# Optimization experiments

Measured on AMD Instinct MI355X. Metric: run time of the kernel, lower is better.

Reference implementation:

```python
import jax, jax.numpy as jnp
import numpy as np

VOCAB = 100000
TAGS = 48
EMB = 256
HID = 512
B, S = 64, 512


def setup_inputs() -> dict:
    key = jax.random.key(0)
    ks = jax.random.split(key, 7)
    sc_e = 1.0 / np.sqrt(EMB)
    sc_h = 1.0 / np.sqrt(HID)
    return {
        "x": jax.random.randint(ks[0], (B, S), 0, VOCAB),
        "emb": jax.random.normal(ks[1], (VOCAB, EMB), jnp.float32),
        "W_ih": jax.random.uniform(ks[2], (4 * HID, EMB), jnp.float32, -sc_e, sc_e),
        "W_hh": jax.random.uniform(ks[3], (4 * HID, HID), jnp.float32, -sc_h, sc_h),
        "b_hh": jax.random.uniform(ks[4], (4 * HID,), jnp.float32, -sc_h, sc_h),
        "fc_W": jax.random.uniform(ks[5], (TAGS, HID), jnp.float32, -sc_h, sc_h),
        "fc_b": jax.random.uniform(ks[6], (TAGS,), jnp.float32, -sc_h, sc_h),
    }


def reference(x, emb, W_ih, W_hh, b_hh, fc_W, fc_b):
    # Embedding lookup: [B,S] -> [B,S,E]
    xe = emb[x]
    # Precompute input projection for all timesteps: [B,S,4H]
    px = jnp.einsum("bse,ge->bsg", xe, W_ih)
    H = W_hh.shape[1]
    Bc = x.shape[0]
    h0 = jnp.zeros((Bc, H), px.dtype)
    c0 = jnp.zeros((Bc, H), px.dtype)

    def step(carry, pxt):
        h, c = carry
        # recurrent dropout prob = 0 -> mask is identity
        gates = pxt + h @ W_hh.T + b_hh  # [B,4H]
        i, f, g, o = jnp.split(gates, 4, axis=-1)
        i = jax.nn.sigmoid(i)
        f = jax.nn.sigmoid(f)
        g = jnp.tanh(g)
        o = jax.nn.sigmoid(o)
        c = f * c + i * g
        h = o * jnp.tanh(c)
        return (h, c), h

    _, hs = jax.lax.scan(step, (h0, c0), jnp.swapaxes(px, 0, 1))
    hs = jnp.swapaxes(hs, 0, 1)  # [B,S,H]
    logits = hs @ fc_W.T + fc_b  # [B,S,TAGS]
    return jax.nn.log_softmax(logits, axis=2)
```

## Files before the change

kernel.cpp:

```cpp
#include <hip/hip_runtime.h>
#include <hip/hip_bf16.h>
#include <hip/hip_fp16.h>

typedef __attribute__((ext_vector_type(8))) short short8;
typedef __attribute__((ext_vector_type(4))) float f32x4;
typedef __attribute__((ext_vector_type(4))) unsigned int u32x4;

#define Hh 512
#define Bb 64
#define Ss 512
#define Gg 2048
#define NROW 32768

static __device__ inline short f2bf(float f) {
    union { float f; unsigned u; } v; v.f = f;
    unsigned r = (v.u + 0x7FFFu + ((v.u >> 16) & 1u)) >> 16;
    return (short)r;
}

static __device__ inline short8 pack_bf8(const float* p) {
    f32x4 u0 = *(const f32x4*)p;
    f32x4 u1 = *(const f32x4*)(p + 4);
    short8 t;
    t[0] = f2bf(u0[0]); t[1] = f2bf(u0[1]); t[2] = f2bf(u0[2]); t[3] = f2bf(u0[3]);
    t[4] = f2bf(u1[0]); t[5] = f2bf(u1[1]); t[6] = f2bf(u1[2]); t[7] = f2bf(u1[3]);
    return t;
}

static __device__ inline float fsigmoid(float x) {
    return __builtin_amdgcn_rcpf(1.f + __builtin_amdgcn_exp2f(x * -1.44269504088896f));
}
static __device__ inline float ftanh(float x) {
    float xc = fminf(fmaxf(x, -15.f), 15.f);
    float e = __builtin_amdgcn_exp2f(xc * 2.88539008177793f);
    return (e - 1.f) / (e + 1.f);
}

__global__ __launch_bounds__(256)
void prep_bf16(const float* __restrict__ wih, const float* __restrict__ fcw,
               short* __restrict__ wih_bf, short* __restrict__ fcw_bf) {
    const int n1 = Gg * 256;
    const int n2 = 48 * Hh;
    for (int i = blockIdx.x * blockDim.x + threadIdx.x; i < n1 + n2;
         i += gridDim.x * blockDim.x) {
        if (i < n1) wih_bf[i] = f2bf(wih[i]);
        else        fcw_bf[i - n1] = f2bf(fcw[i - n1]);
    }
}

__global__ __launch_bounds__(256)
void px_kernel(const int* __restrict__ x, const float* __restrict__ emb,
               const short* __restrict__ wih_bf, const float* __restrict__ bhh,
               _Float16* __restrict__ px) {
    const int w = threadIdx.x >> 6, lane = threadIdx.x & 63;
    const int lr = lane & 15, lc = lane >> 4;
    const int r0 = blockIdx.x * 64 + w * 16;

    short8 a[8];
    const int tok = x[r0 + lr];
    const float* arow = emb + (long)tok * 256;
#pragma unroll
    for (int ks = 0; ks < 8; ks++)
        a[ks] = pack_bf8(arow + ks * 32 + lc * 8);

    for (int g0 = 0; g0 < Gg; g0 += 16) {
        f32x4 acc = {0.f, 0.f, 0.f, 0.f};
#pragma unroll
        for (int ks = 0; ks < 8; ks++) {
            short8 b = *(const short8*)(wih_bf + (g0 + lr) * 256 + ks * 32 + lc * 8);
            acc = __builtin_amdgcn_mfma_f32_16x16x32_bf16(a[ks], b, acc, 0, 0, 0);
        }
        const float bias = bhh[g0 + lr];
#pragma unroll
        for (int i = 0; i < 4; i++) {
            const int r = r0 + lc * 4 + i;
            const int bb = r >> 9, s = r & 511;
            px[((long)s * Bb + bb) * Gg + g0 + lr] = (_Float16)(acc[i] + bias);
        }
    }
}

__global__ __launch_bounds__(512)
void lstm_kernel(const float* __restrict__ whh, const _Float16* __restrict__ px,
                 unsigned int* __restrict__ hbuf32,
                 unsigned int* __restrict__ hs32,
                 int* __restrict__ flags) {
    const int cl  = blockIdx.x & 3;
    const int wgc = blockIdx.x >> 2;
    const int b0 = cl * 16;
    const int J0 = wgc * 64;
    const int tid = threadIdx.x;
    const int w = tid >> 6;
    const int lane = tid & 63;
    const int lr = lane & 15, lc = lane >> 4;
    const int gt = w & 3;
    const int Jsub = (w >> 2) * 32;

    __shared__ float gates[4][16][66];
    __shared__ __align__(16) unsigned int hlds[16 * 256];

    short8 wf[2][16];
#pragma unroll
    for (int u = 0; u < 2; u++)
#pragma unroll
        for (int ks = 0; ks < 16; ks++)
            wf[u][ks] = pack_bf8(whh + (long)(gt * Hh + J0 + Jsub + u * 16 + lr) * Hh + ks * 32 + lc * 8);

    const int eb = tid >> 5;
    const int jp = tid & 31;
    float c0 = 0.f, c1 = 0.f;

    const int gr0 = gt * Hh + J0 + Jsub + lr;

    const int srow = tid >> 5;
    const int scg  = tid & 31;
    const int q0c  = 2 * scg;
    const int chi0 = (q0c ^ ((q0c >> 3) & 7) ^ (srow & 7));
    const int sidx0 = srow * 256 + chi0 * 4;
    const int sidx1 = srow * 256 + (chi0 ^ 1) * 4;

    int* const myflag = flags + cl * 32 + wgc;
    const int* const pollbase = flags + cl * 32;

    float pfA[2][4], pfB[2][4];
#pragma unroll
    for (int u = 0; u < 2; u++)
#pragma unroll
        for (int i = 0; i < 4; i++)
            pfA[u][i] = (float)px[((long)0 * Bb + b0 + lc * 4 + i) * Gg + gr0 + u * 16];

#define LSTM_STEP(T, PFU, PFN)                                                         \
    {                                                                                  \
        const int T_ = (T);                                                            \
        if (T_ == 0) {                                                                 \
            u32x4 z = {0u, 0u, 0u, 0u};                                                \
            *(u32x4*)&hlds[sidx0] = z;                                                 \
            *(u32x4*)&hlds[sidx1] = z;                                                 \
        } else {                                                                       \
            const int* fp = pollbase + (lane & 7);                                     \
            int fv = __hip_atomic_load(fp, __ATOMIC_RELAXED, __HIP_MEMORY_SCOPE_AGENT);\
            while (__any(fv < T_))                                                     \
                fv = __hip_atomic_load(fp, __ATOMIC_RELAXED, __HIP_MEMORY_SCOPE_AGENT);\
            asm volatile("" ::: "memory");                                             \
            const unsigned long long* hb = (const unsigned long long*)                 \
                (hbuf32 + (T_ & 1) * (Bb * Hh / 2) + (b0 + srow) * 256 + scg * 8);     \
            unsigned long long a0 = __hip_atomic_load(hb + 0, __ATOMIC_RELAXED, __HIP_MEMORY_SCOPE_AGENT); \
            unsigned long long a1 = __hip_atomic_load(hb + 1, __ATOMIC_RELAXED, __HIP_MEMORY_SCOPE_AGENT); \
            unsigned long long a2 = __hip_atomic_load(hb + 2, __ATOMIC_RELAXED, __HIP_MEMORY_SCOPE_AGENT); \
            unsigned long long a3 = __hip_atomic_load(hb + 3, __ATOMIC_RELAXED, __HIP_MEMORY_SCOPE_AGENT); \
            u32x4 v0 = {(unsigned)a0, (unsigned)(a0 >> 32), (unsigned)a1, (unsigned)(a1 >> 32)}; \
            u32x4 v1 = {(unsigned)a2, (unsigned)(a2 >> 32), (unsigned)a3, (unsigned)(a3 >> 32)}; \
            *(u32x4*)&hlds[sidx0] = v0;                                                \
            *(u32x4*)&hlds[sidx1] = v1;                                                \
        }                                                                              \
        __syncthreads();                                         \
        f32x4 acc0, acc1;                                                              \
        _Pragma("unroll")                                                              \
        for (int i = 0; i < 4; i++) { acc0[i] = PFU[0][i]; acc1[i] = PFU[1][i]; }      \
        _Pragma("unroll")                                                              \
        for (int ks = 0; ks < 16; ks++) {                                              \
            const int q = ks * 4 + lc;                                                 \
            const int chi = q ^ ((q >> 3) & 7) ^ (lr & 7);                             \
            const short8 af = *(const short8*)&hlds[lr * 256 + chi * 4];               \
            acc0 = __builtin_amdgcn_mfma_f32_16x16x32_bf16(af, wf[0][ks], acc0, 0, 0, 0); \
            acc1 = __builtin_amdgcn_mfma_f32_16x16x32_bf16(af, wf[1][ks], acc1, 0, 0, 0); \
        }                                                                              \
        _Pragma("unroll")                                                              \
        for (int i = 0; i < 4; i++) {                                                  \
            gates[gt][lc * 4 + i][Jsub + lr]      = acc0[i];                           \
            gates[gt][lc * 4 + i][Jsub + 16 + lr] = acc1[i];                           \
        }                                                                              \
        __syncthreads();                                           \
        unsigned hpack;                                                                \
        {                                                                              \
            const float2 gI = *(const float2*)&gates[0][eb][jp * 2];                   \
            const float2 gF = *(const float2*)&gates[1][eb][jp * 2];                   \
            const float2 gG = *(const float2*)&gates[2][eb][jp * 2];                   \
            const float2 gO = *(const float2*)&gates[3][eb][jp * 2];                   \
            c0 = fsigmoid(gF.x) * c0 + fsigmoid(gI.x) * ftanh(gG.x);                   \
            c1 = fsigmoid(gF.y) * c1 + fsigmoid(gI.y) * ftanh(gG.y);                   \
            const float h0 = fsigmoid(gO.x) * ftanh(c0);                               \
            const float h1 = fsigmoid(gO.y) * ftanh(c1);                               \
            hpack = (unsigned)(unsigned short)f2bf(h0)                                 \
                  | ((unsigned)(unsigned short)f2bf(h1) << 16);                        \
            unsigned int* hw = hbuf32 + ((T_ + 1) & 1) * (Bb * Hh / 2)                 \
                               + (b0 + eb) * 256 + (J0 >> 1) + jp;                     \
            __hip_atomic_store(hw, hpack, __ATOMIC_RELAXED, __HIP_MEMORY_SCOPE_AGENT); \
        }                                                                              \
        __syncthreads();          \
        if (tid == 0)                                                                  \
            __hip_atomic_store(myflag, T_ + 1, __ATOMIC_RELAXED, __HIP_MEMORY_SCOPE_AGENT); \
        hs32[((long)(b0 + eb) * Ss + T_) * 256 + (J0 >> 1) + jp] = hpack;              \
        const int tn = (T_ + 1 < Ss) ? T_ + 1 : T_;                                    \
        _Pragma("unroll")                                                              \
        for (int u = 0; u < 2; u++)                                                    \
            _Pragma("unroll")                                                          \
            for (int i = 0; i < 4; i++)                                                \
                PFN[u][i] = (float)px[((long)tn * Bb + b0 + lc * 4 + i) * Gg + gr0 + u * 16]; \
    }

#pragma unroll 1
    for (int t = 0; t < Ss; t += 2) {
        LSTM_STEP(t,     pfA, pfB)
        LSTM_STEP(t + 1, pfB, pfA)
    }
#undef LSTM_STEP
}

__global__ __launch_bounds__(256)
void fc_kernel(const unsigned short* __restrict__ hs, const short* __restrict__ fcw_bf,
               const float* __restrict__ fcb, float* __restrict__ out) {
    const int w = threadIdx.x >> 6, lane = threadIdx.x & 63;
    const int lr = lane & 15, lc = lane >> 4;
    const int r0 = blockIdx.x * 64 + w * 16;

    short8 af[16];
#pragma unroll
    for (int ks = 0; ks < 16; ks++)
        af[ks] = *(const short8*)((const short*)hs + (long)(r0 + lr) * Hh + ks * 32 + lc * 8);

    f32x4 acc[3];
#pragma unroll
    for (int nt = 0; nt < 3; nt++) {
        f32x4 a_ = {0.f, 0.f, 0.f, 0.f};
#pragma unroll
        for (int ks = 0; ks < 16; ks++) {
            short8 b = *(const short8*)(fcw_bf + (nt * 16 + lr) * Hh + ks * 32 + lc * 8);
            a_ = __builtin_amdgcn_mfma_f32_16x16x32_bf16(af[ks], b, a_, 0, 0, 0);
        }
        acc[nt] = a_;
    }

    const float bb0 = fcb[lr], bb1 = fcb[16 + lr], bb2 = fcb[32 + lr];
#pragma unroll
    for (int i = 0; i < 4; i++) {
        float v0 = acc[0][i] + bb0, v1 = acc[1][i] + bb1, v2 = acc[2][i] + bb2;
        float m = fmaxf(v0, fmaxf(v1, v2));
#pragma unroll
        for (int d = 1; d < 16; d <<= 1) m = fmaxf(m, __shfl_xor(m, d));
        float s = expf(v0 - m) + expf(v1 - m) + expf(v2 - m);
#pragma unroll
        for (int d = 1; d < 16; d <<= 1) s += __shfl_xor(s, d);
        const float lse = m + logf(s);
        const long r = r0 + lc * 4 + i;
        out[r * 48 + lr]      = v0 - lse;
        out[r * 48 + 16 + lr] = v1 - lse;
        out[r * 48 + 32 + lr] = v2 - lse;
    }
}

extern "C" void kernel_launch(void* const* d_in, const int* in_sizes, int n_in,
                              void* d_out, int out_size, void* d_ws, size_t ws_size,
                              hipStream_t stream) {
    const int*   x   = (const int*)d_in[0];
    const float* emb = (const float*)d_in[1];
    const float* wih = (const float*)d_in[2];
    const float* whh = (const float*)d_in[3];
    const float* bhh = (const float*)d_in[4];
    const float* fcw = (const float*)d_in[5];
    const float* fcb = (const float*)d_in[6];
    float* out = (float*)d_out;

    char* ws = (char*)d_ws;
    const size_t off_px    = 0;
    const size_t off_hs    = off_px + (size_t)NROW * Gg * 2;
    const size_t off_hbuf  = off_hs + (size_t)NROW * Hh * 2;
    const size_t off_flags = off_hbuf + 2 * (size_t)Bb * Hh * 2;
    const size_t off_wih   = off_flags + 4096;
    const size_t off_fcw   = off_wih + (size_t)Gg * 256 * 2;

    _Float16*     px     = (_Float16*)(ws + off_px);
    unsigned int* hs32   = (unsigned int*)(ws + off_hs);
    unsigned int* hbuf32 = (unsigned int*)(ws + off_hbuf);
    int*          flags  = (int*)(ws + off_flags);
    short*        wih_bf = (short*)(ws + off_wih);
    short*        fcw_bf = (short*)(ws + off_fcw);

    hipMemsetAsync(flags, 0, 4096, stream);
    prep_bf16<<<512, 256, 0, stream>>>(wih, fcw, wih_bf, fcw_bf);
    px_kernel<<<512, 256, 0, stream>>>(x, emb, wih_bf, bhh, px);

    void* args[] = {(void*)&whh, (void*)&px, (void*)&hbuf32, (void*)&hs32, (void*)&flags};
    hipLaunchCooperativeKernel((void*)lstm_kernel, dim3(32), dim3(512), args, 0, stream);

    fc_kernel<<<512, 256, 0, stream>>>((const unsigned short*)hs32, fcw_bf, fcb, out);
}
```

Before: 1.531 ms.

## Fuse input projection into the recurrent LSTM kernel instead of precomputing px

```diff
diff --git a/kernel.cpp b/kernel.cpp
--- a/kernel.cpp
+++ b/kernel.cpp
@@ -37,51 +37,26 @@
 }
 
 __global__ __launch_bounds__(256)
-void prep_bf16(const float* __restrict__ wih, const float* __restrict__ fcw,
-               short* __restrict__ wih_bf, short* __restrict__ fcw_bf) {
-    const int n1 = Gg * 256;
-    const int n2 = 48 * Hh;
-    for (int i = blockIdx.x * blockDim.x + threadIdx.x; i < n1 + n2;
-         i += gridDim.x * blockDim.x) {
-        if (i < n1) wih_bf[i] = f2bf(wih[i]);
-        else        fcw_bf[i - n1] = f2bf(fcw[i - n1]);
-    }
+void prep_fcw(const float* __restrict__ fcw, short* __restrict__ fcw_bf) {
+    const int n = 48 * Hh;
+    for (int i = blockIdx.x * blockDim.x + threadIdx.x; i < n;
+         i += gridDim.x * blockDim.x)
+        fcw_bf[i] = f2bf(fcw[i]);
 }
 
 __global__ __launch_bounds__(256)
-void px_kernel(const int* __restrict__ x, const float* __restrict__ emb,
-               const short* __restrict__ wih_bf, const float* __restrict__ bhh,
-               _Float16* __restrict__ px) {
-    const int w = threadIdx.x >> 6, lane = threadIdx.x & 63;
-    const int lr = lane & 15, lc = lane >> 4;
-    const int r0 = blockIdx.x * 64 + w * 16;
-
-    short8 a[8];
-    const int tok = x[r0 + lr];
-    const float* arow = emb + (long)tok * 256;
-#pragma unroll
-    for (int ks = 0; ks < 8; ks++)
-        a[ks] = pack_bf8(arow + ks * 32 + lc * 8);
-
-    for (int g0 = 0; g0 < Gg; g0 += 16) {
-        f32x4 acc = {0.f, 0.f, 0.f, 0.f};
-#pragma unroll
-        for (int ks = 0; ks < 8; ks++) {
-            short8 b = *(const short8*)(wih_bf + (g0 + lr) * 256 + ks * 32 + lc * 8);
-            acc = __builtin_amdgcn_mfma_f32_16x16x32_bf16(a[ks], b, acc, 0, 0, 0);
-        }
-        const float bias = bhh[g0 + lr];
-#pragma unroll
-        for (int i = 0; i < 4; i++) {
-            const int r = r0 + lc * 4 + i;
-            const int bb = r >> 9, s = r & 511;
-            px[((long)s * Bb + bb) * Gg + g0 + lr] = (_Float16)(acc[i] + bias);
-        }
-    }
+void prep_xe(const int* __restrict__ x, const float* __restrict__ emb,
+             short* __restrict__ xe) {
+    const long i = ((long)blockIdx.x * 256 + threadIdx.x) * 8;
+    const int row = (int)(i >> 8);
+    const int col = (int)(i & 255);
+    const int tok = x[row];
+    *(short8*)(xe + i) = pack_bf8(emb + (long)tok * 256 + col);
 }
 
 __global__ __launch_bounds__(512)
-void lstm_kernel(const float* __restrict__ whh, const _Float16* __restrict__ px,
+void lstm_kernel(const float* __restrict__ whh, const float* __restrict__ wih,
+                 const float* __restrict__ bhh, const short* __restrict__ xe,
                  unsigned int* __restrict__ hbuf32,
                  unsigned int* __restrict__ hs32,
                  int* __restrict__ flags) {
@@ -99,18 +74,27 @@
     __shared__ float gates[4][16][66];
     __shared__ __align__(16) unsigned int hlds[16 * 256];
 
+    const int gr0 = gt * Hh + J0 + Jsub + lr;
+
     short8 wf[2][16];
 #pragma unroll
     for (int u = 0; u < 2; u++)
 #pragma unroll
         for (int ks = 0; ks < 16; ks++)
             wf[u][ks] = pack_bf8(whh + (long)(gt * Hh + J0 + Jsub + u * 16 + lr) * Hh + ks * 32 + lc * 8);
+
+    short8 wif[2][8];
+#pragma unroll
+    for (int u = 0; u < 2; u++)
+#pragma unroll
+        for (int ks = 0; ks < 8; ks++)
+            wif[u][ks] = pack_bf8(wih + (long)(gr0 + u * 16) * 256 + ks * 32 + lc * 8);
+
+    const float bias0 = bhh[gr0], bias1 = bhh[gr0 + 16];
 
     const int eb = tid >> 5;
     const int jp = tid & 31;
     float c0 = 0.f, c1 = 0.f;
-
-    const int gr0 = gt * Hh + J0 + Jsub + lr;
 
     const int srow = tid >> 5;
     const int scg  = tid & 31;
@@ -122,14 +106,24 @@
     int* const myflag = flags + cl * 32 + wgc;
     const int* const pollbase = flags + cl * 32;
 
-    float pfA[2][4], pfB[2][4];
-#pragma unroll
-    for (int u = 0; u < 2; u++)
-#pragma unroll
-        for (int i = 0; i < 4; i++)
-            pfA[u][i] = (float)px[((long)0 * Bb + b0 + lc * 4 + i) * Gg + gr0 + u * 16];
-
-#define LSTM_STEP(T, PFU, PFN)                                                         \
+    const short* const xerow = xe + ((long)(b0 + lr) * Ss) * 256 + lc * 8;
+
+    f32x4 accA0, accA1, accB0, accB1;
+#pragma unroll
+    for (int i = 0; i < 4; i++) { accA0[i] = bias0; accA1[i] = bias1; }
+    {
+        short8 xef[8];
+#pragma unroll
+        for (int ks = 0; ks < 8; ks++)
+            xef[ks] = *(const short8*)(xerow + ks * 32);
+#pragma unroll
+        for (int ks = 0; ks < 8; ks++) {
+            accA0 = __builtin_amdgcn_mfma_f32_16x16x32_bf16(xef[ks], wif[0][ks], accA0, 0, 0, 0);
+            accA1 = __builtin_amdgcn_mfma_f32_16x16x32_bf16(xef[ks], wif[1][ks], accA1, 0, 0, 0);
+        }
+    }
+
+#define LSTM_STEP(T, AC0, AC1, AN0, AN1)                                               \
     {                                                                                  \
         const int T_ = (T);                                                            \
         if (T_ == 0) {                                                                 \
@@ -154,21 +148,18 @@
             *(u32x4*)&hlds[sidx1] = v1;                                                \
         }                                                                              \
         __syncthreads();                                         \
-        f32x4 acc0, acc1;                                                              \
-        _Pragma("unroll")                                                              \
-        for (int i = 0; i < 4; i++) { acc0[i] = PFU[0][i]; acc1[i] = PFU[1][i]; }      \
         _Pragma("unroll")                                                              \
         for (int ks = 0; ks < 16; ks++) {                                              \
             const int q = ks * 4 + lc;                                                 \
             const int chi = q ^ ((q >> 3) & 7) ^ (lr & 7);                             \
             const short8 af = *(const short8*)&hlds[lr * 256 + chi * 4];               \
-            acc0 = __builtin_amdgcn_mfma_f32_16x16x32_bf16(af, wf[0][ks], acc0, 0, 0, 0); \
-            acc1 = __builtin_amdgcn_mfma_f32_16x16x32_bf16(af, wf[1][ks], acc1, 0, 0, 0); \
+            AC0 = __builtin_amdgcn_mfma_f32_16x16x32_bf16(af, wf[0][ks], AC0, 0, 0, 0); \
+            AC1 = __builtin_amdgcn_mfma_f32_16x16x32_bf16(af, wf[1][ks], AC1, 0, 0, 0); \
         }                                                                              \
         _Pragma("unroll")                                                              \
         for (int i = 0; i < 4; i++) {                                                  \
-            gates[gt][lc * 4 + i][Jsub + lr]      = acc0[i];                           \
-            gates[gt][lc * 4 + i][Jsub + 16 + lr] = acc1[i];                           \
+            gates[gt][lc * 4 + i][Jsub + lr]      = AC0[i];                            \
+            gates[gt][lc * 4 + i][Jsub + 16 + lr] = AC1[i];                            \
         }                                                                              \
         __syncthreads();                                           \
         unsigned hpack;                                                                \
@@ -191,18 +182,27 @@
         if (tid == 0)                                                                  \
             __hip_atomic_store(myflag, T_ + 1, __ATOMIC_RELAXED, __HIP_MEMORY_SCOPE_AGENT); \
         hs32[((long)(b0 + eb) * Ss + T_) * 256 + (J0 >> 1) + jp] = hpack;              \
-        const int tn = (T_ + 1 < Ss) ? T_ + 1 : T_;                                    \
-        _Pragma("unroll")                                                              \
-        for (int u = 0; u < 2; u++)                                                    \
+                                \
+        {                                                                              \
+            const int tn = (T_ + 1 < Ss) ? T_ + 1 : T_;                                \
             _Pragma("unroll")                                                          \
-            for (int i = 0; i < 4; i++)                                                \
-                PFN[u][i] = (float)px[((long)tn * Bb + b0 + lc * 4 + i) * Gg + gr0 + u * 16]; \
+            for (int i = 0; i < 4; i++) { AN0[i] = bias0; AN1[i] = bias1; }            \
+            short8 xef[8];                                                             \
+            _Pragma("unroll")                                                          \
+            for (int ks = 0; ks < 8; ks++)                                             \
+                xef[ks] = *(const short8*)(xerow + (long)tn * 256 + ks * 32);          \
+            _Pragma("unroll")                                                          \
+            for (int ks = 0; ks < 8; ks++) {                                           \
+                AN0 = __builtin_amdgcn_mfma_f32_16x16x32_bf16(xef[ks], wif[0][ks], AN0, 0, 0, 0); \
+                AN1 = __builtin_amdgcn_mfma_f32_16x16x32_bf16(xef[ks], wif[1][ks], AN1, 0, 0, 0); \
+            }                                                                          \
+        }                                                                              \
     }
 
 #pragma unroll 1
     for (int t = 0; t < Ss; t += 2) {
-        LSTM_STEP(t,     pfA, pfB)
-        LSTM_STEP(t + 1, pfB, pfA)
+        LSTM_STEP(t,     accA0, accA1, accB0, accB1)
+        LSTM_STEP(t + 1, accB0, accB1, accA0, accA1)
     }
 #undef LSTM_STEP
 }
@@ -262,25 +262,24 @@
     float* out = (float*)d_out;
 
     char* ws = (char*)d_ws;
-    const size_t off_px    = 0;
-    const size_t off_hs    = off_px + (size_t)NROW * Gg * 2;
+    const size_t off_xe    = 0;
+    const size_t off_hs    = (size_t)NROW * Gg * 2;
     const size_t off_hbuf  = off_hs + (size_t)NROW * Hh * 2;
     const size_t off_flags = off_hbuf + 2 * (size_t)Bb * Hh * 2;
-    const size_t off_wih   = off_flags + 4096;
-    const size_t off_fcw   = off_wih + (size_t)Gg * 256 * 2;
-
-    _Float16*     px     = (_Float16*)(ws + off_px);
+    const size_t off_fcw   = off_flags + 4096;
+
+    short*        xe     = (short*)(ws + off_xe);
     unsigned int* hs32   = (unsigned int*)(ws + off_hs);
     unsigned int* hbuf32 = (unsigned int*)(ws + off_hbuf);
     int*          flags  = (int*)(ws + off_flags);
-    short*        wih_bf = (short*)(ws + off_wih);
     short*        fcw_bf = (short*)(ws + off_fcw);
 
     hipMemsetAsync(flags, 0, 4096, stream);
-    prep_bf16<<<512, 256, 0, stream>>>(wih, fcw, wih_bf, fcw_bf);
-    px_kernel<<<512, 256, 0, stream>>>(x, emb, wih_bf, bhh, px);
-
-    void* args[] = {(void*)&whh, (void*)&px, (void*)&hbuf32, (void*)&hs32, (void*)&flags};
+    prep_fcw<<<96, 256, 0, stream>>>(fcw, fcw_bf);
+    prep_xe<<<4096, 256, 0, stream>>>(x, emb, xe);
+
+    void* args[] = {(void*)&whh, (void*)&wih, (void*)&bhh, (void*)&xe,
+                    (void*)&hbuf32, (void*)&hs32, (void*)&flags};
     hipLaunchCooperativeKernel((void*)lstm_kernel, dim3(32), dim3(512), args, 0, stream);
 
     fc_kernel<<<512, 256, 0, stream>>>((const unsigned short*)hs32, fcw_bf, fcb, out);
```

After: 3.262 ms. 2.13x slower.

## Fuse input projection into LSTM kernel as producer blocks overlapping recurrence

Applied to the files above, without the earlier changes.

```diff
diff --git a/kernel.cpp b/kernel.cpp
--- a/kernel.cpp
+++ b/kernel.cpp
@@ -25,6 +25,18 @@
     t[0] = f2bf(u0[0]); t[1] = f2bf(u0[1]); t[2] = f2bf(u0[2]); t[3] = f2bf(u0[3]);
     t[4] = f2bf(u1[0]); t[5] = f2bf(u1[1]); t[6] = f2bf(u1[2]); t[7] = f2bf(u1[3]);
     return t;
+}
+
+static __device__ inline unsigned long long pack4f16(f32x4 v) {
+    union { _Float16 h[4]; unsigned long long q; } u;
+    u.h[0] = (_Float16)v[0]; u.h[1] = (_Float16)v[1];
+    u.h[2] = (_Float16)v[2]; u.h[3] = (_Float16)v[3];
+    return u.q;
+}
+static __device__ inline void unpack4f16(unsigned long long q, float* o) {
+    union { unsigned long long q; _Float16 h[4]; } u; u.q = q;
+    o[0] = (float)u.h[0]; o[1] = (float)u.h[1];
+    o[2] = (float)u.h[2]; o[3] = (float)u.h[3];
 }
 
 static __device__ inline float fsigmoid(float x) {
@@ -48,53 +60,66 @@
     }
 }
 
-__global__ __launch_bounds__(256)
-void px_kernel(const int* __restrict__ x, const float* __restrict__ emb,
-               const short* __restrict__ wih_bf, const float* __restrict__ bhh,
-               _Float16* __restrict__ px) {
-    const int w = threadIdx.x >> 6, lane = threadIdx.x & 63;
-    const int lr = lane & 15, lc = lane >> 4;
-    const int r0 = blockIdx.x * 64 + w * 16;
-
-    short8 a[8];
-    const int tok = x[r0 + lr];
-    const float* arow = emb + (long)tok * 256;
-#pragma unroll
-    for (int ks = 0; ks < 8; ks++)
-        a[ks] = pack_bf8(arow + ks * 32 + lc * 8);
-
-    for (int g0 = 0; g0 < Gg; g0 += 16) {
-        f32x4 acc = {0.f, 0.f, 0.f, 0.f};
-#pragma unroll
-        for (int ks = 0; ks < 8; ks++) {
-            short8 b = *(const short8*)(wih_bf + (g0 + lr) * 256 + ks * 32 + lc * 8);
-            acc = __builtin_amdgcn_mfma_f32_16x16x32_bf16(a[ks], b, acc, 0, 0, 0);
-        }
-        const float bias = bhh[g0 + lr];
-#pragma unroll
-        for (int i = 0; i < 4; i++) {
-            const int r = r0 + lc * 4 + i;
-            const int bb = r >> 9, s = r & 511;
-            px[((long)s * Bb + bb) * Gg + g0 + lr] = (_Float16)(acc[i] + bias);
-        }
-    }
-}
-
 __global__ __launch_bounds__(512)
-void lstm_kernel(const float* __restrict__ whh, const _Float16* __restrict__ px,
-                 unsigned int* __restrict__ hbuf32,
-                 unsigned int* __restrict__ hs32,
-                 int* __restrict__ flags) {
-    const int cl  = blockIdx.x & 3;
-    const int wgc = blockIdx.x >> 2;
-    const int b0 = cl * 16;
-    const int J0 = wgc * 64;
+void lstm_fused(const float* __restrict__ whh, const int* __restrict__ x,
+                const float* __restrict__ emb, const short* __restrict__ wih_bf,
+                const float* __restrict__ bhh,
+                unsigned long long* __restrict__ px3,
+                unsigned int* __restrict__ hbuf32,
+                unsigned int* __restrict__ hs32,
+                int* __restrict__ flags) {
     const int tid = threadIdx.x;
     const int w = tid >> 6;
     const int lane = tid & 63;
     const int lr = lane & 15, lc = lane >> 4;
     const int gt = w & 3;
     const int Jsub = (w >> 2) * 32;
+    int* const pxflag = flags + 128;
+
+    if (blockIdx.x >= 32) {
+        const int p = blockIdx.x - 32;
+        const int colb = gt * Hh + Jsub + lr;
+        for (int t = p; t < Ss; t += 32) {
+            for (int cl = 0; cl < 4; cl++) {
+                const int b0 = cl * 16;
+                const int tok = x[(b0 + lr) * Ss + t];
+                const float* arow = emb + (long)tok * 256;
+                short8 a[8];
+#pragma unroll
+                for (int ks = 0; ks < 8; ks++)
+                    a[ks] = pack_bf8(arow + ks * 32 + lc * 8);
+                for (int wgc = 0; wgc < 8; wgc++) {
+                    const int cb = colb + wgc * 64;
+                    f32x4 acc0, acc1;
+                    const float bi0 = bhh[cb], bi1 = bhh[cb + 16];
+#pragma unroll
+                    for (int i = 0; i < 4; i++) { acc0[i] = bi0; acc1[i] = bi1; }
+#pragma unroll
+                    for (int ks = 0; ks < 8; ks++) {
+                        const short8 bf0 = *(const short8*)(wih_bf + (long)cb * 256 + ks * 32 + lc * 8);
+                        const short8 bf1 = *(const short8*)(wih_bf + (long)(cb + 16) * 256 + ks * 32 + lc * 8);
+                        acc0 = __builtin_amdgcn_mfma_f32_16x16x32_bf16(a[ks], bf0, acc0, 0, 0, 0);
+                        acc1 = __builtin_amdgcn_mfma_f32_16x16x32_bf16(a[ks], bf1, acc1, 0, 0, 0);
+                    }
+                    const long base = ((((long)t * 4 + cl) * 8 + wgc) * 8 + w) * 64 + lane;
+                    __hip_atomic_store(px3 + base * 2,     pack4f16(acc0),
+                                       __ATOMIC_RELAXED, __HIP_MEMORY_SCOPE_AGENT);
+                    __hip_atomic_store(px3 + base * 2 + 1, pack4f16(acc1),
+                                       __ATOMIC_RELAXED, __HIP_MEMORY_SCOPE_AGENT);
+                }
+            }
+            asm volatile("s_waitcnt vmcnt(0)" ::: "memory");
+            __syncthreads();
+            if (tid == 0)
+                __hip_atomic_store(&pxflag[t], 1, __ATOMIC_RELAXED, __HIP_MEMORY_SCOPE_AGENT);
+        }
+        return;
+    }
+
+    const int cl  = blockIdx.x & 3;
+    const int wgc = blockIdx.x >> 2;
+    const int b0 = cl * 16;
+    const int J0 = wgc * 64;
 
     __shared__ float gates[4][16][66];
     __shared__ __align__(16) unsigned int hlds[16 * 256];
@@ -109,8 +134,6 @@
     const int eb = tid >> 5;
     const int jp = tid & 31;
     float c0 = 0.f, c1 = 0.f;
-
-    const int gr0 = gt * Hh + J0 + Jsub + lr;
 
     const int srow = tid >> 5;
     const int scg  = tid & 31;
@@ -121,13 +144,19 @@
 
     int* const myflag = flags + cl * 32 + wgc;
     const int* const pollbase = flags + cl * 32;
+    const long pbase0 = (((long)cl * 8 + wgc) * 8 + w) * 64 + lane;
 
     float pfA[2][4], pfB[2][4];
-#pragma unroll
-    for (int u = 0; u < 2; u++)
-#pragma unroll
-        for (int i = 0; i < 4; i++)
-            pfA[u][i] = (float)px[((long)0 * Bb + b0 + lc * 4 + i) * Gg + gr0 + u * 16];
+    {
+        int pv;
+        do { pv = __hip_atomic_load(&pxflag[0], __ATOMIC_RELAXED, __HIP_MEMORY_SCOPE_AGENT); }
+        while (pv == 0);
+        asm volatile("" ::: "memory");
+        unsigned long long qa = __hip_atomic_load(px3 + pbase0 * 2,     __ATOMIC_RELAXED, __HIP_MEMORY_SCOPE_AGENT);
+        unsigned long long qb = __hip_atomic_load(px3 + pbase0 * 2 + 1, __ATOMIC_RELAXED, __HIP_MEMORY_SCOPE_AGENT);
+        unpack4f16(qa, pfA[0]);
+        unpack4f16(qb, pfA[1]);
+    }
 
 #define LSTM_STEP(T, PFU, PFN)                                                         \
     {                                                                                  \
@@ -191,12 +220,19 @@
         if (tid == 0)                                                                  \
             __hip_atomic_store(myflag, T_ + 1, __ATOMIC_RELAXED, __HIP_MEMORY_SCOPE_AGENT); \
         hs32[((long)(b0 + eb) * Ss + T_) * 256 + (J0 >> 1) + jp] = hpack;              \
-        const int tn = (T_ + 1 < Ss) ? T_ + 1 : T_;                                    \
-        _Pragma("unroll")                                                              \
-        for (int u = 0; u < 2; u++)                                                    \
-            _Pragma("unroll")                                                          \
-            for (int i = 0; i < 4; i++)                                                \
-                PFN[u][i] = (float)px[((long)tn * Bb + b0 + lc * 4 + i) * Gg + gr0 + u * 16]; \
+                   \
+        {                                                                              \
+            const int tn = (T_ + 1 < Ss) ? T_ + 1 : T_;                                \
+            int pv;                                                                    \
+            do { pv = __hip_atomic_load(&pxflag[tn], __ATOMIC_RELAXED, __HIP_MEMORY_SCOPE_AGENT); } \
+            while (pv == 0);                                                           \
+            asm volatile("" ::: "memory");                                             \
+            const long pb = pbase0 + (long)tn * 16384;                                 \
+            unsigned long long qa = __hip_atomic_load(px3 + pb * 2,     __ATOMIC_RELAXED, __HIP_MEMORY_SCOPE_AGENT); \
+            unsigned long long qb = __hip_atomic_load(px3 + pb * 2 + 1, __ATOMIC_RELAXED, __HIP_MEMORY_SCOPE_AGENT); \
+            unpack4f16(qa, PFN[0]);                                                    \
+            unpack4f16(qb, PFN[1]);                                                    \
+        }                                                                              \
     }
 
 #pragma unroll 1
@@ -262,26 +298,26 @@
     float* out = (float*)d_out;
 
     char* ws = (char*)d_ws;
-    const size_t off_px    = 0;
-    const size_t off_hs    = off_px + (size_t)NROW * Gg * 2;
+    const size_t off_px3   = 0;
+    const size_t off_hs    = off_px3 + (size_t)NROW * Gg * 2;
     const size_t off_hbuf  = off_hs + (size_t)NROW * Hh * 2;
     const size_t off_flags = off_hbuf + 2 * (size_t)Bb * Hh * 2;
     const size_t off_wih   = off_flags + 4096;
     const size_t off_fcw   = off_wih + (size_t)Gg * 256 * 2;
 
-    _Float16*     px     = (_Float16*)(ws + off_px);
-    unsigned int* hs32   = (unsigned int*)(ws + off_hs);
-    unsigned int* hbuf32 = (unsigned int*)(ws + off_hbuf);
-    int*          flags  = (int*)(ws + off_flags);
-    short*        wih_bf = (short*)(ws + off_wih);
-    short*        fcw_bf = (short*)(ws + off_fcw);
+    unsigned long long* px3    = (unsigned long long*)(ws + off_px3);
+    unsigned int*       hs32   = (unsigned int*)(ws + off_hs);
+    unsigned int*       hbuf32 = (unsigned int*)(ws + off_hbuf);
+    int*                flags  = (int*)(ws + off_flags);
+    short*              wih_bf = (short*)(ws + off_wih);
+    short*              fcw_bf = (short*)(ws + off_fcw);
 
     hipMemsetAsync(flags, 0, 4096, stream);
     prep_bf16<<<512, 256, 0, stream>>>(wih, fcw, wih_bf, fcw_bf);
-    px_kernel<<<512, 256, 0, stream>>>(x, emb, wih_bf, bhh, px);
-
-    void* args[] = {(void*)&whh, (void*)&px, (void*)&hbuf32, (void*)&hs32, (void*)&flags};
-    hipLaunchCooperativeKernel((void*)lstm_kernel, dim3(32), dim3(512), args, 0, stream);
+
+    void* args[] = {(void*)&whh, (void*)&x, (void*)&emb, (void*)&wih_bf, (void*)&bhh,
+                    (void*)&px3, (void*)&hbuf32, (void*)&hs32, (void*)&flags};
+    hipLaunchCooperativeKernel((void*)lstm_fused, dim3(64), dim3(512), args, 0, stream);
 
     fc_kernel<<<512, 256, 0, stream>>>((const unsigned short*)hs32, fcw_bf, fcb, out);
 }
```

Measured after the change: 2.224 ms. +45.3%, slower.
